# Performance work log

Hardware: AMD Instinct MI355X
Metric: run time of the kernel (lower is better)

Reference implementation:

```python
import jax, jax.numpy as jnp
import numpy as np
import math

B, HID, T, D = 4, 1024, 2048, 1024
NEG_INF = -2.0**15 + 1.0  # matches torch constant -32767.0


def setup_inputs() -> dict:
    key = jax.random.key(0)
    ks = jax.random.split(key, 9)
    s = 0.02
    return {
        "minibatch": jax.random.normal(ks[0], (B, HID, T), dtype=jnp.float32),
        "emb_w": jax.random.normal(ks[1], (D, HID), dtype=jnp.float32) * s,
        "emb_b": jax.random.normal(ks[2], (D,), dtype=jnp.float32) * s,
        "key_w": jax.random.normal(ks[3], (D, D), dtype=jnp.float32) * s,
        "key_b": jax.random.normal(ks[4], (D,), dtype=jnp.float32) * s,
        "query_w": jax.random.normal(ks[5], (D, D), dtype=jnp.float32) * s,
        "query_b": jax.random.normal(ks[6], (D,), dtype=jnp.float32) * s,
        "value_w": jax.random.normal(ks[7], (D, D), dtype=jnp.float32) * s,
        "value_b": jax.random.normal(ks[8], (D,), dtype=jnp.float32) * s,
    }


def reference(minibatch, emb_w, emb_b, key_w, key_b, query_w, query_b, value_w, value_b):
    # minibatch: [B, hidden, T] -> permute -> [B, T, hidden]
    x = jnp.transpose(minibatch, (0, 2, 1))
    m = x @ emb_w.T + emb_b                      # [B, T, D]
    keys = m @ key_w.T + key_b                   # [B, T, D]
    queries = m @ query_w.T + query_b            # [B, T, D]
    values = m @ value_w.T + value_b             # [B, T, D]
    logits = jnp.einsum('btd,bsd->bts', queries, keys)  # [B, T, T]
    mask = jnp.tril(jnp.ones((logits.shape[1], logits.shape[2]), dtype=bool))
    logits = jnp.where(mask[None], logits, jnp.float32(NEG_INF))
    # NOTE: original code applies softmax over dim=1 (query axis) and divides
    # by sqrt(d_model) AFTER the softmax — reproduced faithfully here.
    probs = jax.nn.softmax(logits, axis=1) / jnp.float32(math.sqrt(D))
    read = jnp.einsum('bts,bsd->btd', probs, values)     # [B, T, D]
    out = read + m
    return jnp.transpose(out, (0, 2, 1))                  # [B, D, T]
```

## Files before the change

### kernel.cpp

```cpp
#include <hip/hip_runtime.h>

#define T_DIM 2048
#define D_DIM 1024
#define H_DIM 1024
#define B_DIM 4

typedef __attribute__((ext_vector_type(8))) __bf16 bf16x8;
typedef __attribute__((ext_vector_type(4))) float f32x4;
typedef __attribute__((ext_vector_type(8))) unsigned short us8;

__device__ __forceinline__ unsigned short f2b(float f) {
  union { float f; unsigned int u; } x; x.f = f;
  unsigned int r = x.u + 0x7fffu + ((x.u >> 16) & 1u);
  return (unsigned short)(r >> 16);
}
__device__ __forceinline__ float b2f(unsigned short b) {
  union { unsigned int u; float f; } x; x.u = ((unsigned int)b) << 16;
  return x.f;
}

__device__ __forceinline__ void async16(unsigned short* l, const unsigned short* g) {
  __builtin_amdgcn_global_load_lds((const __attribute__((address_space(1))) void*)g,
                                   (__attribute__((address_space(3))) void*)l,
                                   16, 0, 0);
}

__global__ __launch_bounds__(256) void prep_kernel(const float* __restrict__ ew,
                                                   const float* __restrict__ kw,
                                                   const float* __restrict__ qw,
                                                   const float* __restrict__ vw,
                                                   const float* __restrict__ kb,
                                                   const float* __restrict__ qb,
                                                   const float* __restrict__ vb,
                                                   unsigned short* __restrict__ oe,
                                                   unsigned short* __restrict__ okqv,
                                                   float* __restrict__ ob) {
  int bid = blockIdx.x;
  if (bid == 4096) {
    #pragma unroll
    for (int k = 0; k < 3; k++) {
      int f4 = threadIdx.x + k * 256;
      int fi = f4 * 4;
      const float* src = fi < 1024 ? kb + fi : (fi < 2048 ? qb + (fi - 1024) : vb + (fi - 2048));
      *(float4*)(&ob[fi]) = *(const float4*)src;
    }
    return;
  }
  int i = bid * 256 + threadIdx.x;
  int seg = i >> 18;
  int off = i & 262143;
  const float* in = seg == 0 ? ew : (seg == 1 ? kw : (seg == 2 ? qw : vw));
  unsigned short* out = seg == 0 ? oe : okqv + (size_t)(seg - 1) * 1048576;
  float4 v = ((const float4*)in)[off];
  ushort4 o;
  o.x = f2b(v.x); o.y = f2b(v.y); o.z = f2b(v.z); o.w = f2b(v.w);
  ((ushort4*)out)[off] = o;
}

__global__ __launch_bounds__(256) void transpose_f32_kernel(const float* __restrict__ in,
                                                            unsigned short* __restrict__ out,
                                                            int inLD, size_t sIn, int R, size_t sOut) {
  __shared__ float tile[32][33];
  int c0 = blockIdx.x * 32, r0 = blockIdx.y * 32;
  int tx = threadIdx.x & 31, ty = threadIdx.x >> 5;
  const float* I = in + (size_t)blockIdx.z * sIn;
  #pragma unroll
  for (int i = 0; i < 32; i += 8)
    tile[ty + i][tx] = I[(size_t)(r0 + ty + i) * inLD + (c0 + tx)];
  __syncthreads();
  unsigned short* O = out + (size_t)blockIdx.z * sOut;
  #pragma unroll
  for (int i = 0; i < 32; i += 8)
    O[(size_t)(c0 + ty + i) * R + (r0 + tx)] = f2b(tile[tx][ty + i]);
}

#define BAR_ asm volatile("s_barrier" ::: "memory")
#define VM8_ asm volatile("s_waitcnt vmcnt(8)" ::: "memory")
#define VM6_ asm volatile("s_waitcnt vmcnt(6)" ::: "memory")
#define VM4_ asm volatile("s_waitcnt vmcnt(4)" ::: "memory")
#define VM0_ asm volatile("s_waitcnt vmcnt(0)" ::: "memory")

#define FRG(base, row, ks) \
  (*(const bf16x8*)((base) + (row) * 64 + ((((ks) << 2) | hi) ^ (lo & 7)) * 8))

#define STGA3(t, bb, u) async16(smem + (bb) * 24576 + (u) * 4096 + tid * 8, \
                                A + (size_t)((u) * 64 + rl0) * lda + (t) * 64 + ce)
#define STGB3(t, bb, u) async16(smem + (bb) * 24576 + 8192 + (u) * 4096 + tid * 8, \
                                Bm + (size_t)((u) * 64 + rl0) * ldb + (t) * 64 + ce)
#define STGTILE(t, bb) do { STGA3(t, bb, 0); STGA3(t, bb, 1); \
    STGB3(t, bb, 0); STGB3(t, bb, 1); STGB3(t, bb, 2); STGB3(t, bb, 3); } while (0)

#define LOADFRAGS(bA, bB)                                            \
  _Pragma("unroll") for (int m_ = 0; m_ < 4; m_++) {                 \
    af[m_][0] = FRG(bA, wr * 64 + m_ * 16 + lo, 0);                  \
    af[m_][1] = FRG(bA, wr * 64 + m_ * 16 + lo, 1);                  \
  }                                                                  \
  _Pragma("unroll") for (int n_ = 0; n_ < 4; n_++) {                 \
    bg[n_][0] = FRG(bB, wc * 64 + n_ * 16 + lo, 0);                  \
    bg[n_][1] = FRG(bB, wc * 64 + n_ * 16 + lo, 1);                  \
  }

#define MFMA32_                                                          \
  __builtin_amdgcn_s_setprio(1);                                         \
  _Pragma("unroll") for (int ks_ = 0; ks_ < 2; ks_++)                    \
    _Pragma("unroll") for (int m_ = 0; m_ < 4; m_++)                     \
      _Pragma("unroll") for (int n_ = 0; n_ < 4; n_++)                   \
        acc[m_][n_] = __builtin_amdgcn_mfma_f32_16x16x32_bf16(           \
            af[m_][ks_], bg[n_][ks_], acc[m_][n_], 0, 0, 0);             \
  __builtin_amdgcn_s_setprio(0);

template <int OMODE>
__global__ __launch_bounds__(512, 2)
void gemm8_kernel(const unsigned short* __restrict__ A,
                  const unsigned short* __restrict__ Bm,
                  const float* __restrict__ bias,
                  unsigned short* __restrict__ Cb,
                  int N, int K, int lda, int ldb) {
  __shared__ __align__(16) unsigned short smem[73728];

  int gx = gridDim.x;
  int nwg = gx * gridDim.y;
  int flat = blockIdx.x + gx * blockIdx.y;
  int cpx = nwg >> 3;
  int f2 = (flat & 7) * cpx + (flat >> 3);
  int bn = f2 % gx, bm = f2 / gx;

  A  += (size_t)bm * 128 * lda;
  Bm += (size_t)bn * 256 * ldb;

  int tid = threadIdx.x;
  int lane = tid & 63, wid = tid >> 6;
  int wr = wid >> 2, wc = wid & 3;
  int lo = lane & 15, hi = lane >> 4;
  int rl0 = tid >> 3;
  int ce = 8 * ((tid & 7) ^ (rl0 & 7));

  int nt = K / 64;

  bf16x8 af[4][2], bg[4][2];
  f32x4 acc[4][4] = {};

  STGTILE(0, 0);
  STGTILE(1, 1);
  VM6_; BAR_;

  int cur = 0;
  for (int t = 0; t < nt - 2; t++) {
    const unsigned short* bA = smem + cur * 24576;
    const unsigned short* bB = bA + 8192;
    LOADFRAGS(bA, bB)
    int b2 = cur + 2; if (b2 >= 3) b2 -= 3;
    STGTILE(t + 2, b2);
    MFMA32_
    VM6_; BAR_;
    cur = (cur + 1 == 3) ? 0 : cur + 1;
  }
  {
    const unsigned short* bA = smem + cur * 24576;
    const unsigned short* bB = bA + 8192;
    LOADFRAGS(bA, bB)
    MFMA32_
    VM0_; BAR_;
    cur = (cur + 1 == 3) ? 0 : cur + 1;
  }
  {
    const unsigned short* bA = smem + cur * 24576;
    const unsigned short* bB = bA + 8192;
    LOADFRAGS(bA, bB)
    MFMA32_
  }

  __syncthreads();
  int row0 = bm * 128, col0 = bn * 256;
  unsigned short* ep = smem;
  #pragma unroll
  for (int n = 0; n < 4; n++) {
    int cl = wc * 64 + n * 16 + lo;
    float bvc = (OMODE == 1) ? bias[col0 + cl] : 0.f;
    #pragma unroll
    for (int m = 0; m < 4; m++) {
      int rl = wr * 64 + m * 16 + hi * 4;
      #pragma unroll
      for (int j = 0; j < 4; j++) {
        float bv = (OMODE == 3) ? bias[row0 + rl + j] : bvc;
        ep[(rl + j) * 264 + cl] = f2b(acc[m][n][j] + bv);
      }
    }
  }
  __syncthreads();
  #pragma unroll
  for (int it = 0; it < 8; it++) {
    int idx = it * 512 + tid, r = idx >> 5, c = idx & 31;
    *(uint4*)(Cb + (size_t)(row0 + r) * N + col0 + c * 8) =
        *(const uint4*)(ep + r * 264 + c * 8);
  }
}

#define STGAH(t, h) do { \
    unsigned short* d_ = ldsA + ((t) & 1) * 16384 + (h) * 8192 + tid * 8;            \
    const unsigned short* s_ = A + (size_t)((h) * 128 + rl0) * lda + (t) * 64 + ce;  \
    async16(d_, s_); async16(d_ + 4096, s_ + (size_t)64 * lda); } while (0)
#define STGBH(t, h) do { \
    unsigned short* d_ = ldsB + ((t) & 1) * 16384 + (h) * 8192 + tid * 8;            \
    const unsigned short* s_ = Bm + (size_t)((h) * 128 + rl0) * ldb + (t) * 64 + ce; \
    async16(d_, s_); async16(d_ + 4096, s_ + (size_t)64 * ldb); } while (0)

#define LDA_(bA, mb)                                                   \
  _Pragma("unroll") for (int m_ = 0; m_ < 4; m_++) {                   \
    int row_ = wr * 128 + ((mb) + m_) * 16 + lo;                       \
    af[m_][0] = FRG(bA, row_, 0);                                      \
    af[m_][1] = FRG(bA, row_, 1);                                      \
  }

#define LDB_(bB, nb, bgv)                                              \
  _Pragma("unroll") for (int n_ = 0; n_ < 2; n_++) {                   \
    int row_ = wc * 64 + ((nb) + n_) * 16 + lo;                        \
    bgv[n_][0] = FRG(bB, row_, 0);                                     \
    bgv[n_][1] = FRG(bB, row_, 1);                                     \
  }

#define MM_(mb, nb, bgv)                                                             \
  __builtin_amdgcn_s_setprio(1);                                                     \
  _Pragma("unroll") for (int m_ = 0; m_ < 4; m_++)                                   \
    _Pragma("unroll") for (int n_ = 0; n_ < 2; n_++) {                               \
      acc[(mb) + m_][(nb) + n_] = __builtin_amdgcn_mfma_f32_16x16x32_bf16(           \
          af[m_][0], bgv[n_][0], acc[(mb) + m_][(nb) + n_], 0, 0, 0);                \
      acc[(mb) + m_][(nb) + n_] = __builtin_amdgcn_mfma_f32_16x16x32_bf16(           \
          af[m_][1], bgv[n_][1], acc[(mb) + m_][(nb) + n_], 0, 0, 0);                \
    }                                                                                \
  __builtin_amdgcn_s_setprio(0);

template <bool BIAS, bool SKIP>
__global__ __launch_bounds__(512, 2)
void gemmL_kernel(const unsigned short* __restrict__ A,
                  const unsigned short* __restrict__ Bm,
                  const float* __restrict__ bias,
                  unsigned short* __restrict__ Cb,
                  int N, int K, int lda, int ldb,
                  size_t sAb, size_t sBb, size_t sCb) {
  __shared__ __align__(16) unsigned short smem[65536];
  unsigned short* ldsA = smem;
  unsigned short* ldsB = smem + 32768;

  int gx = gridDim.x;
  int nwg = gx * gridDim.y;
  int flat = blockIdx.x + gx * blockIdx.y;
  int cpx = nwg >> 3;
  int f2x = (flat & 7) * cpx + (flat >> 3);
  int bn = f2x % gx, bm = f2x / gx;
  int bz = blockIdx.z;
  if (SKIP && bn < bm) return;

  A  += (size_t)bz * sAb + (size_t)bm * 256 * lda;
  Bm += (size_t)bz * sBb + (size_t)bn * 256 * ldb;

  int tid = threadIdx.x;
  int lane = tid & 63, wid = tid >> 6;
  int wr = wid >> 2, wc = wid & 3;
  int lo = lane & 15, hi = lane >> 4;
  int rl0 = tid >> 3;
  int ce = 8 * ((tid & 7) ^ (rl0 & 7));

  int nt = K / 64;

  bf16x8 af[4][2], bg0[2][2], bg1[2][2];
  f32x4 acc[8][4] = {};

  STGAH(0, 0); STGAH(0, 1); STGBH(0, 0); STGBH(0, 1);
  STGAH(1, 0); STGAH(1, 1); STGBH(1, 0); STGBH(1, 1);
  VM8_; BAR_;

  const unsigned short* bA0 = ldsA;
  const unsigned short* bB0 = ldsB;
  const unsigned short* bA1 = ldsA + 16384;
  const unsigned short* bB1 = ldsB + 16384;

  int nIter = nt >> 1;
  for (int i = 0; i < nIter; i++) {
    bool last = (i == nIter - 1);
    int ta = 2 * i, tb = ta + 1;
    LDA_(bA0, 0) LDB_(bB0, 0, bg0)
    BAR_; MM_(0, 0, bg0) BAR_;
    LDB_(bB0, 2, bg1)
    BAR_; MM_(0, 2, bg1) BAR_;
    LDA_(bA0, 4)
    if (!last) STGBH(ta + 2, 0);
    BAR_; MM_(4, 0, bg0) BAR_;
    if (!last) { STGAH(ta + 2, 0); STGBH(ta + 2, 1); }
    BAR_; MM_(4, 2, bg1)
    if (last) { VM0_; } else { VM6_; }
    BAR_;
    LDA_(bA1, 0) LDB_(bB1, 0, bg0)
    if (!last) STGAH(ta + 2, 1);
    BAR_; MM_(0, 0, bg0) BAR_;
    LDB_(bB1, 2, bg1)
    BAR_; MM_(0, 2, bg1) BAR_;
    LDA_(bA1, 4)
    if (!last) STGBH(tb + 2, 0);
    BAR_; MM_(4, 0, bg0) BAR_;
    if (!last) { STGAH(tb + 2, 0); STGBH(tb + 2, 1); STGAH(tb + 2, 1); }
    BAR_; MM_(4, 2, bg1)
    if (!last) VM8_;
    BAR_;
  }

  __syncthreads();
  int row0 = bm * 256, col0 = bn * 256;
  size_t coff = (size_t)bz * sCb;
  unsigned short* ep = smem;
  #pragma unroll
  for (int half = 0; half < 2; half++) {
    __syncthreads();
    if (wr == half) {
      #pragma unroll
      for (int n = 0; n < 4; n++) {
        int cl = wc * 64 + n * 16 + lo;
        float bv = BIAS ? bias[col0 + cl] : 0.f;
        #pragma unroll
        for (int m = 0; m < 8; m++) {
          int rl = m * 16 + hi * 4;
          #pragma unroll
          for (int j = 0; j < 4; j++)
            ep[(rl + j) * 264 + cl] = f2b(acc[m][n][j] + bv);
        }
      }
    }
    __syncthreads();
    #pragma unroll
    for (int it = 0; it < 8; it++) {
      int idx = it * 512 + tid, r = idx >> 5, c = idx & 31;
      *(uint4*)(Cb + coff + (size_t)(row0 + half * 128 + r) * N + col0 + c * 8) =
          *(const uint4*)(ep + r * 264 + c * 8);
    }
  }
}

#define PSTGA(t, bb, u) async16(smem + (bb) * 16384 + (u) * 4096 + tid * 8, \
                                Ap + (size_t)((u) * 64 + rl0) * T_DIM + (t) * 64 + ce)
#define PSTGB(t, bb, u) async16(smem + (bb) * 16384 + 8192 + (u) * 4096 + tid * 8, \
                                Bp + (size_t)((u) * 64 + rl0) * 8192 + (t) * 64 + ce)
#define PSTG(t, bb) do { PSTGA(t, bb, 0); PSTGA(t, bb, 1); \
                         PSTGB(t, bb, 0); PSTGB(t, bb, 1); } while (0)

#define PVFRAGS(bA, bB)                                              \
  _Pragma("unroll") for (int m_ = 0; m_ < 4; m_++) {                 \
    af[m_][0] = FRG(bA, wr * 64 + m_ * 16 + lo, 0);                  \
    af[m_][1] = FRG(bA, wr * 64 + m_ * 16 + lo, 1);                  \
  }                                                                  \
  _Pragma("unroll") for (int n_ = 0; n_ < 2; n_++) {                 \
    bg[n_][0] = FRG(bB, wc * 32 + n_ * 16 + lo, 0);                  \
    bg[n_][1] = FRG(bB, wc * 32 + n_ * 16 + lo, 1);                  \
  }

#define PVMFMA_                                                          \
  __builtin_amdgcn_s_setprio(1);                                         \
  _Pragma("unroll") for (int ks_ = 0; ks_ < 2; ks_++)                    \
    _Pragma("unroll") for (int m_ = 0; m_ < 4; m_++)                     \
      _Pragma("unroll") for (int n_ = 0; n_ < 2; n_++)                   \
        acc[m_][n_] = __builtin_amdgcn_mfma_f32_16x16x32_bf16(           \
            af[m_][ks_], bg[n_][ks_], acc[m_][n_], 0, 0, 0);             \
  __builtin_amdgcn_s_setprio(0);

__global__ __launch_bounds__(512, 2)
void pv_kernel(const unsigned short* __restrict__ probs,
               const unsigned short* __restrict__ VTd,
               const unsigned short* __restrict__ mres,
               float* __restrict__ out) {
  __shared__ __align__(16) unsigned short smem[49152];
  int bn = blockIdx.x;
  int jj = blockIdx.y;
  int bz = blockIdx.z;
  int tid = threadIdx.x;
  int lane = tid & 63, wid = tid >> 6;
  int wr = wid >> 2, wc = wid & 3;
  int lo = lane & 15, hi = lane >> 4;
  int rl0 = tid >> 3;
  int ce = 8 * ((tid & 7) ^ (rl0 & 7));

  const unsigned short* Bp = VTd + (size_t)(bn * 128) * 8192 + bz * T_DIM;

  #pragma unroll 1
  for (int seg = 0; seg < 2; seg++) {
    int jt = (seg == 0) ? jj : (15 - jj);
    int nt = ((seg == 0) ? (jj + 1) : (16 - jj)) * 2;
    const unsigned short* Ap = probs + (size_t)bz * T_DIM * T_DIM + (size_t)(jt * 128) * T_DIM;

    bf16x8 af[4][2], bg[2][2];
    f32x4 acc[4][2] = {};

    PSTG(0, 0);
    PSTG(1, 1);
    VM4_; BAR_;

    int cur = 0;
    for (int t = 0; t < nt - 2; t++) {
      const unsigned short* bA = smem + cur * 16384;
      const unsigned short* bB = bA + 8192;
      PVFRAGS(bA, bB)
      int b2 = cur + 2; if (b2 >= 3) b2 -= 3;
      PSTG(t + 2, b2);
      PVMFMA_
      VM4_; BAR_;
      cur = (cur + 1 == 3) ? 0 : cur + 1;
    }
    {
      const unsigned short* bA = smem + cur * 16384;
      const unsigned short* bB = bA + 8192;
      PVFRAGS(bA, bB)
      PVMFMA_
      VM0_; BAR_;
      cur = (cur + 1 == 3) ? 0 : cur + 1;
    }
    {
      const unsigned short* bA = smem + cur * 16384;
      const unsigned short* bB = bA + 8192;
      PVFRAGS(bA, bB)
      PVMFMA_
    }

    __syncthreads();
    float* ep = (float*)smem;
    #pragma unroll
    for (int n = 0; n < 2; n++) {
      int dl = wc * 32 + n * 16 + lo;
      #pragma unroll
      for (int m = 0; m < 4; m++) {
        int tl = wr * 64 + m * 16 + hi * 4;
        #pragma unroll
        for (int j = 0; j < 4; j++) {
          float v = acc[m][n][j] +
              b2f(mres[((size_t)bz * T_DIM + jt * 128 + tl + j) * D_DIM + bn * 128 + dl]);
          ep[dl * 132 + tl + j] = v;
        }
      }
    }
    __syncthreads();
    #pragma unroll
    for (int it = 0; it < 8; it++) {
      int idx = it * 512 + tid, r = idx >> 5, c = idx & 31;
      *(float4*)(out + ((size_t)bz * D_DIM + bn * 128 + r) * T_DIM + jt * 128 + c * 4) =
          *(const float4*)(ep + r * 132 + c * 4);
    }
    __syncthreads();
  }
}

__device__ __forceinline__ float wred_max(float v) {
  #pragma unroll
  for (int o = 32; o > 0; o >>= 1) v = fmaxf(v, __shfl_down(v, o, 64));
  return v;
}
__device__ __forceinline__ float wred_sum(float v) {
  #pragma unroll
  for (int o = 32; o > 0; o >>= 1) v += __shfl_down(v, o, 64);
  return v;
}

__global__ __launch_bounds__(256) void softmax_stats_kernel(const unsigned short* __restrict__ lg,
                                                            float* __restrict__ smax,
                                                            float* __restrict__ sinv) {
  __shared__ float sb[4];
  int row = blockIdx.x;
  int s = row & (T_DIM - 1);
  us8 v = ((const us8*)(lg + (size_t)row * T_DIM))[threadIdx.x];
  int tb = threadIdx.x * 8;
  float x[8];
  float mx = -3.4e38f;
  #pragma unroll
  for (int j = 0; j < 8; j++) {
    x[j] = (tb + j >= s) ? b2f(v[j]) : -3.4e38f;
    mx = fmaxf(mx, x[j]);
  }
  mx = wred_max(mx);
  if ((threadIdx.x & 63) == 0) sb[threadIdx.x >> 6] = mx;
  __syncthreads();
  mx = fmaxf(fmaxf(sb[0], sb[1]), fmaxf(sb[2], sb[3]));
  __syncthreads();
  float sum = 0.f;
  #pragma unroll
  for (int j = 0; j < 8; j++) sum += __expf(x[j] - mx);
  sum = wred_sum(sum);
  if ((threadIdx.x & 63) == 0) sb[threadIdx.x >> 6] = sum;
  __syncthreads();
  if (threadIdx.x == 0) {
    float tot = sb[0] + sb[1] + sb[2] + sb[3];
    smax[row] = mx;
    sinv[row] = 1.0f / (tot * 32.0f);
  }
}

__global__ __launch_bounds__(256) void probs_kernel(const unsigned short* __restrict__ lg,
                                                    const float* __restrict__ smax,
                                                    const float* __restrict__ sinv,
                                                    unsigned short* __restrict__ probs) {
  int bz = blockIdx.z;
  int t0 = blockIdx.x * 32, s0 = blockIdx.y * 32;
  if (s0 >= (((t0 >> 7) + 1) << 7)) return;
  __shared__ unsigned short tile[32][33];
  int tx = threadIdx.x & 31, ty = threadIdx.x >> 5;
  const unsigned short* L = lg + (size_t)bz * T_DIM * T_DIM;
  #pragma unroll
  for (int i = 0; i < 32; i += 8)
    tile[ty + i][tx] = L[(size_t)(s0 + ty + i) * T_DIM + (t0 + tx)];
  __syncthreads();
  unsigned short* P = probs + (size_t)bz * T_DIM * T_DIM;
  #pragma unroll
  for (int i = 0; i < 32; i += 8) {
    int t = t0 + ty + i, s = s0 + tx;
    float x = b2f(tile[tx][ty + i]);
    float p = (t >= s) ? __expf(x - smax[bz * T_DIM + s]) * sinv[bz * T_DIM + s] : 0.f;
    P[(size_t)t * T_DIM + s] = f2b(p);
  }
}

extern "C" void kernel_launch(void* const* d_in, const int* in_sizes, int n_in,
                              void* d_out, int out_size, void* d_ws, size_t ws_size,
                              hipStream_t stream) {
  const float* minibatch = (const float*)d_in[0];
  const float* emb_w   = (const float*)d_in[1];
  const float* emb_b   = (const float*)d_in[2];
  const float* key_w   = (const float*)d_in[3];
  const float* key_b   = (const float*)d_in[4];
  const float* query_w = (const float*)d_in[5];
  const float* query_b = (const float*)d_in[6];
  const float* value_w = (const float*)d_in[7];
  const float* value_b = (const float*)d_in[8];
  float* out = (float*)d_out;

  char* ws = (char*)d_ws;
  const size_t MB = 1ull << 20;
  unsigned short* wbf_emb = (unsigned short*)(ws + 0 * MB);
  unsigned short* wbf_kqv = (unsigned short*)(ws + 2 * MB);
  float*          kqv_b   = (float*)(ws + 8 * MB);
  unsigned short* m_bf    = (unsigned short*)(ws + 9 * MB);
  unsigned short* KQ      = (unsigned short*)(ws + 25 * MB);
  unsigned short* VTd     = (unsigned short*)(ws + 57 * MB);
  unsigned short* logits_bf = (unsigned short*)(ws + 89 * MB);
  unsigned short* xT      = (unsigned short*)(ws + 153 * MB);
  unsigned short* probs   = (unsigned short*)(ws + 153 * MB);
  float*          smax    = (float*)(ws + 186 * MB);
  float*          sinv    = (float*)(ws + 186 * MB + 32768);

  const int BT = B_DIM * T_DIM;
  const size_t TT = (size_t)T_DIM * T_DIM;

  prep_kernel<<<4097, 256, 0, stream>>>(emb_w, key_w, query_w, value_w,
                                        key_b, query_b, value_b,
                                        wbf_emb, wbf_kqv, kqv_b);

  transpose_f32_kernel<<<dim3(T_DIM / 32, H_DIM / 32, B_DIM), 256, 0, stream>>>(
      minibatch, xT, T_DIM, (size_t)H_DIM * T_DIM, H_DIM, (size_t)T_DIM * H_DIM);

  gemm8_kernel<1><<<dim3(D_DIM / 256, BT / 128, 1), 512, 0, stream>>>(
      xT, wbf_emb, emb_b, m_bf, D_DIM, H_DIM, H_DIM, H_DIM);

  gemmL_kernel<true, false><<<dim3(2048 / 256, BT / 256, 1), 512, 0, stream>>>(
      m_bf, wbf_kqv, kqv_b, KQ, 2048, D_DIM, D_DIM, D_DIM, 0, 0, 0);

  gemm8_kernel<3><<<dim3(BT / 256, D_DIM / 128, 1), 512, 0, stream>>>(
      wbf_kqv + 2 * 1024 * 1024, m_bf, value_b, VTd, BT, D_DIM, D_DIM, D_DIM);

  gemmL_kernel<false, true><<<dim3(T_DIM / 256, T_DIM / 256, B_DIM), 512, 0, stream>>>(
      KQ, KQ + 1024, nullptr, logits_bf, T_DIM, D_DIM, 2048, 2048,
      (size_t)T_DIM * 2048, (size_t)T_DIM * 2048, TT);

  softmax_stats_kernel<<<BT, 256, 0, stream>>>(logits_bf, smax, sinv);

  probs_kernel<<<dim3(T_DIM / 32, T_DIM / 32, B_DIM), 256, 0, stream>>>(
      logits_bf, smax, sinv, probs);

  pv_kernel<<<dim3(8, 8, B_DIM), 512, 0, stream>>>(probs, VTd, m_bf, out);
}
```

Before: 194.8 us.

## Widen PV tile to 256 columns and skip masked logits in softmax stats

The probs@V kernel now covers 256 output columns per block instead of 128. It stages four V sub-tiles per stage and reuses the shared macros LOADFRAGS/MFMA32_ with a 4x4 accumulator per wave, so each probs tile is loaded half as often. The grid drops to 4x8x4 blocks, which is fewer blocks in flight, and shared memory per block grows. Separately, the softmax stats kernel now reads only the unmasked tail of each row, from s rounded down to 256 onward, which skips loads of masked logits.

```diff
diff --git a/kernel.cpp b/kernel.cpp
--- a/kernel.cpp
+++ b/kernel.cpp
@@ -335,39 +335,20 @@
   }
 }
 
-#define PSTGA(t, bb, u) async16(smem + (bb) * 16384 + (u) * 4096 + tid * 8, \
-                                Ap + (size_t)((u) * 64 + rl0) * T_DIM + (t) * 64 + ce)
-#define PSTGB(t, bb, u) async16(smem + (bb) * 16384 + 8192 + (u) * 4096 + tid * 8, \
+#define QSTGA(t, bb, u) async16(smem + (bb) * 24576 + (u) * 4096 + tid * 8, \
+                                Ap + (size_t)((u) * 64 + rl0) * 2048 + (t) * 64 + ce)
+#define QSTGB(t, bb, u) async16(smem + (bb) * 24576 + 8192 + (u) * 4096 + tid * 8, \
                                 Bp + (size_t)((u) * 64 + rl0) * 8192 + (t) * 64 + ce)
-#define PSTG(t, bb) do { PSTGA(t, bb, 0); PSTGA(t, bb, 1); \
-                         PSTGB(t, bb, 0); PSTGB(t, bb, 1); } while (0)
-
-#define PVFRAGS(bA, bB)                                              \
-  _Pragma("unroll") for (int m_ = 0; m_ < 4; m_++) {                 \
-    af[m_][0] = FRG(bA, wr * 64 + m_ * 16 + lo, 0);                  \
-    af[m_][1] = FRG(bA, wr * 64 + m_ * 16 + lo, 1);                  \
-  }                                                                  \
-  _Pragma("unroll") for (int n_ = 0; n_ < 2; n_++) {                 \
-    bg[n_][0] = FRG(bB, wc * 32 + n_ * 16 + lo, 0);                  \
-    bg[n_][1] = FRG(bB, wc * 32 + n_ * 16 + lo, 1);                  \
-  }
-
-#define PVMFMA_                                                          \
-  __builtin_amdgcn_s_setprio(1);                                         \
-  _Pragma("unroll") for (int ks_ = 0; ks_ < 2; ks_++)                    \
-    _Pragma("unroll") for (int m_ = 0; m_ < 4; m_++)                     \
-      _Pragma("unroll") for (int n_ = 0; n_ < 2; n_++)                   \
-        acc[m_][n_] = __builtin_amdgcn_mfma_f32_16x16x32_bf16(           \
-            af[m_][ks_], bg[n_][ks_], acc[m_][n_], 0, 0, 0);             \
-  __builtin_amdgcn_s_setprio(0);
+#define QSTG(t, bb) do { QSTGA(t, bb, 0); QSTGA(t, bb, 1); \
+    QSTGB(t, bb, 0); QSTGB(t, bb, 1); QSTGB(t, bb, 2); QSTGB(t, bb, 3); } while (0)
 
 __global__ __launch_bounds__(512, 2)
 void pv_kernel(const unsigned short* __restrict__ probs,
                const unsigned short* __restrict__ VTd,
                const unsigned short* __restrict__ mres,
                float* __restrict__ out) {
-  __shared__ __align__(16) unsigned short smem[49152];
-  int bn = blockIdx.x;
+  __shared__ __align__(16) unsigned short smem[73728];
+  int bd = blockIdx.x;
   int jj = blockIdx.y;
   int bz = blockIdx.z;
   int tid = threadIdx.x;
@@ -377,7 +358,7 @@
   int rl0 = tid >> 3;
   int ce = 8 * ((tid & 7) ^ (rl0 & 7));
 
-  const unsigned short* Bp = VTd + (size_t)(bn * 128) * 8192 + bz * T_DIM;
+  const unsigned short* Bp = VTd + (size_t)(bd * 256) * 8192 + bz * T_DIM;
 
   #pragma unroll 1
   for (int seg = 0; seg < 2; seg++) {
@@ -385,60 +366,60 @@
     int nt = ((seg == 0) ? (jj + 1) : (16 - jj)) * 2;
     const unsigned short* Ap = probs + (size_t)bz * T_DIM * T_DIM + (size_t)(jt * 128) * T_DIM;
 
-    bf16x8 af[4][2], bg[2][2];
-    f32x4 acc[4][2] = {};
-
-    PSTG(0, 0);
-    PSTG(1, 1);
-    VM4_; BAR_;
+    bf16x8 af[4][2], bg[4][2];
+    f32x4 acc[4][4] = {};
+
+    QSTG(0, 0);
+    QSTG(1, 1);
+    VM6_; BAR_;
 
     int cur = 0;
     for (int t = 0; t < nt - 2; t++) {
-      const unsigned short* bA = smem + cur * 16384;
+      const unsigned short* bA = smem + cur * 24576;
       const unsigned short* bB = bA + 8192;
-      PVFRAGS(bA, bB)
+      LOADFRAGS(bA, bB)
       int b2 = cur + 2; if (b2 >= 3) b2 -= 3;
-      PSTG(t + 2, b2);
-      PVMFMA_
-      VM4_; BAR_;
+      QSTG(t + 2, b2);
+      MFMA32_
+      VM6_; BAR_;
       cur = (cur + 1 == 3) ? 0 : cur + 1;
     }
     {
-      const unsigned short* bA = smem + cur * 16384;
+      const unsigned short* bA = smem + cur * 24576;
       const unsigned short* bB = bA + 8192;
-      PVFRAGS(bA, bB)
-      PVMFMA_
+      LOADFRAGS(bA, bB)
+      MFMA32_
       VM0_; BAR_;
       cur = (cur + 1 == 3) ? 0 : cur + 1;
     }
     {
-      const unsigned short* bA = smem + cur * 16384;
+      const unsigned short* bA = smem + cur * 24576;
       const unsigned short* bB = bA + 8192;
-      PVFRAGS(bA, bB)
-      PVMFMA_
+      LOADFRAGS(bA, bB)
+      MFMA32_
     }
 
     __syncthreads();
     float* ep = (float*)smem;
     #pragma unroll
-    for (int n = 0; n < 2; n++) {
-      int dl = wc * 32 + n * 16 + lo;
+    for (int n = 0; n < 4; n++) {
+      int dl = wc * 64 + n * 16 + lo;
       #pragma unroll
       for (int m = 0; m < 4; m++) {
         int tl = wr * 64 + m * 16 + hi * 4;
         #pragma unroll
         for (int j = 0; j < 4; j++) {
           float v = acc[m][n][j] +
-              b2f(mres[((size_t)bz * T_DIM + jt * 128 + tl + j) * D_DIM + bn * 128 + dl]);
+              b2f(mres[((size_t)bz * T_DIM + jt * 128 + tl + j) * D_DIM + bd * 256 + dl]);
           ep[dl * 132 + tl + j] = v;
         }
       }
     }
     __syncthreads();
     #pragma unroll
-    for (int it = 0; it < 8; it++) {
+    for (int it = 0; it < 16; it++) {
       int idx = it * 512 + tid, r = idx >> 5, c = idx & 31;
-      *(float4*)(out + ((size_t)bz * D_DIM + bn * 128 + r) * T_DIM + jt * 128 + c * 4) =
+      *(float4*)(out + ((size_t)bz * D_DIM + bd * 256 + r) * T_DIM + jt * 128 + c * 4) =
           *(const float4*)(ep + r * 132 + c * 4);
     }
     __syncthreads();
@@ -462,14 +443,21 @@
   __shared__ float sb[4];
   int row = blockIdx.x;
   int s = row & (T_DIM - 1);
-  us8 v = ((const us8*)(lg + (size_t)row * T_DIM))[threadIdx.x];
-  int tb = threadIdx.x * 8;
+  int t0 = s & ~255;
+  int n8 = (T_DIM - t0) >> 3;
   float x[8];
   float mx = -3.4e38f;
-  #pragma unroll
-  for (int j = 0; j < 8; j++) {
-    x[j] = (tb + j >= s) ? b2f(v[j]) : -3.4e38f;
-    mx = fmaxf(mx, x[j]);
+  if (threadIdx.x < n8) {
+    us8 v = ((const us8*)(lg + (size_t)row * T_DIM + t0))[threadIdx.x];
+    int tb = t0 + threadIdx.x * 8;
+    #pragma unroll
+    for (int j = 0; j < 8; j++) {
+      x[j] = (tb + j >= s) ? b2f(v[j]) : -3.4e38f;
+      mx = fmaxf(mx, x[j]);
+    }
+  } else {
+    #pragma unroll
+    for (int j = 0; j < 8; j++) x[j] = -3.4e38f;
   }
   mx = wred_max(mx);
   if ((threadIdx.x & 63) == 0) sb[threadIdx.x >> 6] = mx;
@@ -569,5 +557,5 @@
   probs_kernel<<<dim3(T_DIM / 32, T_DIM / 32, B_DIM), 256, 0, stream>>>(
       logits_bf, smax, sinv, probs);
 
-  pv_kernel<<<dim3(8, 8, B_DIM), 512, 0, stream>>>(probs, VTd, m_bf, out);
-}
+  pv_kernel<<<dim3(4, 8, B_DIM), 512, 0, stream>>>(probs, VTd, m_bf, out);
+}
```

After: 199.4 us. 1.02x slower.
